# Kernel optimization log

Measured on AMD Instinct MI355X. Metric: run time of the kernel, lower is better.

Reference implementation:

```python
import jax, jax.numpy as jnp
import numpy as np

B, N, M = 2, 2048, 2048
D_K, D_V, H = 256, 256, 8
D_KS = D_K // H  # 32, per-head key dim (ceil(256/8))
D_VS = D_V // H  # 32
MASK_BIG = 1e32


def setup_inputs() -> dict:
    key = jax.random.key(0)
    ks = jax.random.split(key, 10)
    s = 0.02
    queries = jax.random.normal(ks[0], (B, N, D_K), jnp.float32)
    keys_ = jax.random.normal(ks[1], (B, M, D_K), jnp.float32)
    values = jax.random.normal(ks[2], (B, M, D_V), jnp.float32)
    presence = (jax.random.uniform(ks[3], (B, M)) > 0.3).astype(jnp.float32)
    Wq = jax.random.normal(ks[4], (D_K, D_KS * H), jnp.float32) * s
    bq = jnp.zeros((D_KS * H,), jnp.float32)
    Wk = jax.random.normal(ks[5], (D_K, D_KS * H), jnp.float32) * s
    bk = jnp.zeros((D_KS * H,), jnp.float32)
    Wv = jax.random.normal(ks[6], (D_V, D_VS * H), jnp.float32) * s
    bv = jnp.zeros((D_VS * H,), jnp.float32)
    Wo = jax.random.normal(ks[7], (D_VS * H, D_V), jnp.float32) * s
    bo = jnp.zeros((D_V,), jnp.float32)
    return {"queries": queries, "keys": keys_, "values": values, "presence": presence,
            "Wq": Wq, "bq": bq, "Wk": Wk, "bk": bk, "Wv": Wv, "bv": bv, "Wo": Wo, "bo": bo}


def reference(queries, keys, values, presence, Wq, bq, Wk, bk, Wv, bv, Wo, bo):
    # Project and split into heads. torch's split(d_k_s,-1)+cat(...,0) puts the
    # head index as the outer batch dim; a [B,N,H,d] reshape is the same math.
    q = (queries @ Wq + bq).reshape(B, N, H, D_KS)
    k = (keys @ Wk + bk).reshape(B, M, H, D_KS)
    v = (values @ Wv + bv).reshape(B, M, H, D_VS)
    # Raw scores, additive presence mask, then scale by sqrt(per-head d_k)
    scores = jnp.einsum('bnhd,bmhd->bhnm', q, k)
    scores = scores - (1.0 - presence)[:, None, None, :] * MASK_BIG
    attn = jax.nn.softmax(scores / np.sqrt(D_KS).astype(np.float32), axis=-1)
    o = jnp.einsum('bhnm,bmhd->bnhd', attn, v).reshape(B, N, H * D_VS)
    return o @ Wo + bo
```

## Files before the change

kernel.cpp:

```cpp
#include <hip/hip_runtime.h>

#define B_ 2
#define N_ 2048
#define M_ 2048
#define D_ 256
#define H_ 8
#define DH_ 32
#define SPLITS 2
#define QSCALE (0.17677669529663689f * 1.4426950408889634f)

typedef __attribute__((ext_vector_type(8))) short short8;
typedef __attribute__((ext_vector_type(4))) float f32x4;
typedef unsigned short u16;
typedef unsigned int u32;

#if __has_builtin(__builtin_amdgcn_exp2f)
#define EXP2 __builtin_amdgcn_exp2f
#else
#define EXP2 exp2f
#endif

__device__ __forceinline__ u16 f2bf(float f) {
  u32 u = __float_as_uint(f);
  return (u16)((u + 0x7fffu + ((u >> 16) & 1u)) >> 16);
}
__device__ __forceinline__ u32 cvtpk_bf16(float lo, float hi) {
  u32 r;
  asm("v_cvt_pk_bf16_f32 %0, %1, %2" : "=v"(r) : "v"(lo), "v"(hi));
  return r;
}
__device__ __forceinline__ void gload_lds16(const u16* g, u16* l) {
  __builtin_amdgcn_global_load_lds((const __attribute__((address_space(1))) void*)g,
                                   (__attribute__((address_space(3))) void*)l, 16, 0, 0);
}

__global__ __launch_bounds__(256, 2) void qkvproj_kernel(
    const float* __restrict__ Xq, const float* __restrict__ Xk, const float* __restrict__ Xv,
    const float* __restrict__ Wq, const float* __restrict__ Wk, const float* __restrict__ Wv,
    const float* __restrict__ bq, const float* __restrict__ bk, const float* __restrict__ bv,
    u16* __restrict__ qb, u16* __restrict__ kb, u16* __restrict__ vtb) {
  __shared__ u16 wsT[64 * 256];
  __shared__ u16 xs[64 * 256];
  const int p = blockIdx.y;
  const int nb = blockIdx.x & 63, cb = blockIdx.x >> 6;
  const int n0B = nb * 64, c0B = cb * 64;
  const float* X = p == 0 ? Xq : (p == 1 ? Xk : Xv);
  const float* W = p == 0 ? Wq : (p == 1 ? Wk : Wv);
  const float* bias = p == 0 ? bq : (p == 1 ? bk : bv);
  const int t = threadIdx.x;

  {
    const int cL = (t & 15) * 4, kB = (t >> 4) * 16;
    const float* wp = W + (size_t)kB * D_ + c0B + cL;
#pragma unroll
    for (int u = 0; u < 4; ++u) {
      const int k0 = kB + 4 * u;
      const f32x4 w0 = *(const f32x4*)(wp + (size_t)(4 * u + 0) * D_);
      const f32x4 w1 = *(const f32x4*)(wp + (size_t)(4 * u + 1) * D_);
      const f32x4 w2 = *(const f32x4*)(wp + (size_t)(4 * u + 2) * D_);
      const f32x4 w3 = *(const f32x4*)(wp + (size_t)(4 * u + 3) * D_);
#pragma unroll
      for (int cc = 0; cc < 4; ++cc) {
        const int c = cL + cc;
        uint2 v;
        v.x = cvtpk_bf16(w0[cc], w1[cc]);
        v.y = cvtpk_bf16(w2[cc], w3[cc]);
        *(uint2*)(wsT + c * 256 + (((k0 >> 3) ^ (c & 7)) * 8) + (k0 & 7)) = v;
      }
    }
  }
  {
    const int nL = t >> 2, k64 = (t & 3) * 64;
    const float* xp = X + (size_t)(n0B + nL) * D_ + k64;
#pragma unroll
    for (int m = 0; m < 8; ++m) {
      const f32x4 a = *(const f32x4*)(xp + 8 * m);
      const f32x4 b = *(const f32x4*)(xp + 8 * m + 4);
      uint4 v;
      v.x = cvtpk_bf16(a[0], a[1]);
      v.y = cvtpk_bf16(a[2], a[3]);
      v.z = cvtpk_bf16(b[0], b[1]);
      v.w = cvtpk_bf16(b[2], b[3]);
      const int k0 = k64 + 8 * m;
      *(uint4*)(xs + nL * 256 + (((k0 >> 3) ^ (nL & 7)) * 8)) = v;
    }
  }
  __syncthreads();

  const int wv = t >> 6, lane = t & 63, lr = lane & 15, lg = lane >> 4;
  const f32x4 zz = {0.f, 0.f, 0.f, 0.f};
  f32x4 acc[4] = {zz, zz, zz, zz};
  const int arow = wv * 16 + lr;
#pragma unroll
  for (int ks = 0; ks < 8; ++ks) {
    const short8 a = *(const short8*)(wsT + arow * 256 + (((ks * 4 + lg) ^ (arow & 7)) * 8));
#pragma unroll
    for (int ng = 0; ng < 4; ++ng) {
      const int brow = ng * 16 + lr;
      const short8 b = *(const short8*)(xs + brow * 256 + (((ks * 4 + lg) ^ (brow & 7)) * 8));
      acc[ng] = __builtin_amdgcn_mfma_f32_16x16x32_bf16(a, b, acc[ng], 0, 0, 0);
    }
  }

  const int cg4 = c0B + wv * 16 + lg * 4;
  const f32x4 bias4 = *(const f32x4*)(bias + cg4);
  if (p < 2) {
    u16* ob = p == 0 ? qb : kb;
    const float sc = p == 0 ? QSCALE : 1.0f;
#pragma unroll
    for (int ng = 0; ng < 4; ++ng) {
      const int n = n0B + ng * 16 + lr;
      const int b = n >> 11, nn = n & (N_ - 1);
#pragma unroll
      for (int j = 0; j < 4; ++j) {
        const int c = cg4 + j;
        ob[((size_t)(b * H_ + (c >> 5)) * N_ + nn) * DH_ + (c & 31)] =
            f2bf((acc[ng][j] + bias4[j]) * sc);
      }
    }
  } else {
#pragma unroll
    for (int ng = 0; ng < 4; ++ng) {
      const int n = n0B + ng * 16 + lr;
      const int b = n >> 11, nn = n & (M_ - 1);
#pragma unroll
      for (int j = 0; j < 4; ++j) {
        const int c = cg4 + j;
        vtb[((size_t)(b * H_ + (c >> 5)) * DH_ + (c & 31)) * M_ + nn] =
            f2bf(acc[ng][j] + bias4[j]);
      }
    }
  }
}

__global__ __launch_bounds__(256, 4) void attn_kernel(
    const u16* __restrict__ qb, const u16* __restrict__ kb,
    const u16* __restrict__ vtb, const float* __restrict__ presence,
    float* __restrict__ opart, float* __restrict__ lpart) {
  __shared__ u16 kvlds[2][4096];
  __shared__ u16 plds[4][1024];
  const int t = threadIdx.x;
  const int wv = t >> 6, lane = t & 63;
  const int lr = lane & 15, lg = lane >> 4;
  const int s = blockIdx.x >> 9;
  const int bh = (blockIdx.x >> 5) & 15;
  const int qblk = blockIdx.x & 31;
  const int b = bh >> 3, h = bh & 7;
  const int n0 = qblk * 64 + wv * 16;
  const int m0 = s * (M_ / SPLITS);
  const int NI = (M_ / SPLITS) / 64;

  const int gsk = (t & 3) ^ ((t >> 3) & 3);
  const u16* kst = kb + ((size_t)bh * M_ + m0 + (t >> 2)) * DH_ + gsk * 8;
  const int gsv = (t & 7) ^ ((t >> 3) & 7);
  const u16* vst = vtb + ((size_t)bh * DH_ + (t >> 3)) * M_ + m0 + gsv * 8;
  u16* const ldswK = &kvlds[0][0] + wv * 512;
  u16* const ldswV = &kvlds[0][0] + 2048 + wv * 512;

  const int ko0 = lr * 32 + (lg ^ ((lr >> 1) & 3)) * 8;
  const int sw = lr & 7;
  const int vo0 = (lg ^ sw) * 8;
  const int vo1 = ((4 + lg) ^ sw) * 8;

  const short8 qf = *(const short8*)(qb + ((size_t)bh * N_ + n0 + lr) * DH_ + lg * 8);
  const float* pbase = presence + (size_t)b * M_ + m0 + lg * 4;
  u16* const plw = plds[wv] + lr * 64;

  const f32x4 zz = {0.f, 0.f, 0.f, 0.f};
  f32x4 o0 = zz, o1 = zz, racc = zz;

  gload_lds16(kst, ldswK);
  gload_lds16(vst, ldswV);
  __syncthreads();

#pragma unroll 2
  for (int i = 0; i < NI; ++i) {
    const int mm = i * 64;
    const u16* kl = &kvlds[i & 1][0];
    const u16* vl = &kvlds[i & 1][2048];
    f32x4 pr[4];
#pragma unroll
    for (int tt = 0; tt < 4; ++tt) pr[tt] = *(const f32x4*)(pbase + mm + tt * 16);
    if (i + 1 < NI) {
      const int bo = ((i + 1) & 1) * 4096;
      gload_lds16(kst + (size_t)(i + 1) * (64 * DH_), ldswK + bo);
      gload_lds16(vst + (size_t)(i + 1) * 64, ldswV + bo);
    }

    f32x4 s4[4];
    __builtin_amdgcn_s_setprio(1);
#pragma unroll
    for (int tt = 0; tt < 4; ++tt) {
      const short8 kf = *(const short8*)(kl + tt * 512 + ko0);
      s4[tt] = __builtin_amdgcn_mfma_f32_16x16x32_bf16(kf, qf, zz, 0, 0, 0);
    }
    __builtin_amdgcn_s_setprio(0);

#pragma unroll
    for (int tt = 0; tt < 4; ++tt) {
      s4[tt] += (pr[tt] - 1.f) * 1e30f;
#pragma unroll
      for (int j = 0; j < 4; ++j) s4[tt][j] = EXP2(s4[tt][j]);
      racc += s4[tt];
      const int slot = (2 * tt + (lg >> 1)) ^ sw;
      *(uint2*)(plw + slot * 8 + (lg & 1) * 4) =
          make_uint2(cvtpk_bf16(s4[tt][0], s4[tt][1]), cvtpk_bf16(s4[tt][2], s4[tt][3]));
    }
    const short8 pf0 = *(const short8*)(plw + vo0);
    const short8 pf1 = *(const short8*)(plw + vo1);
    const short8 vf0 = *(const short8*)(vl + lr * 64 + vo0);
    const short8 vf1 = *(const short8*)(vl + lr * 64 + vo1);
    const short8 vf2 = *(const short8*)(vl + (16 + lr) * 64 + vo0);
    const short8 vf3 = *(const short8*)(vl + (16 + lr) * 64 + vo1);
    __builtin_amdgcn_s_setprio(1);
    o0 = __builtin_amdgcn_mfma_f32_16x16x32_bf16(pf0, vf0, o0, 0, 0, 0);
    o0 = __builtin_amdgcn_mfma_f32_16x16x32_bf16(pf1, vf1, o0, 0, 0, 0);
    o1 = __builtin_amdgcn_mfma_f32_16x16x32_bf16(pf0, vf2, o1, 0, 0, 0);
    o1 = __builtin_amdgcn_mfma_f32_16x16x32_bf16(pf1, vf3, o1, 0, 0, 0);
    __builtin_amdgcn_s_setprio(0);
    __syncthreads();
  }

  float l = (racc[0] + racc[1]) + (racc[2] + racc[3]);
  l += __shfl_xor(l, 16);
  l += __shfl_xor(l, 32);
  if (lg == 0) lpart[((size_t)s * (B_ * N_) + b * N_ + n0 + lr) * H_ + h] = l;

  float* ob = opart + ((size_t)s * (B_ * N_) + (size_t)b * N_ + n0) * D_ + h * DH_;
#pragma unroll
  for (int j = 0; j < 4; ++j) {
    const int q = lg * 4 + j;
    ob[(size_t)q * D_ + lr] = o0[j];
    ob[(size_t)q * D_ + 16 + lr] = o1[j];
  }
}

__global__ __launch_bounds__(256, 2) void projo_kernel(
    const float* __restrict__ opart, const float* __restrict__ lpart,
    const float* __restrict__ Wo, const float* __restrict__ bo,
    float* __restrict__ out) {
  __shared__ u16 wsT[64 * 256];
  __shared__ u16 xs[64 * 256];
  const int nb = blockIdx.x & 63, cb = blockIdx.x >> 6;
  const int n0B = nb * 64, c0B = cb * 64;
  const int t = threadIdx.x;

  {
    const int cL = (t & 15) * 4, kB = (t >> 4) * 16;
    const float* wp = Wo + (size_t)kB * D_ + c0B + cL;
#pragma unroll
    for (int u = 0; u < 4; ++u) {
      const int k0 = kB + 4 * u;
      const f32x4 w0 = *(const f32x4*)(wp + (size_t)(4 * u + 0) * D_);
      const f32x4 w1 = *(const f32x4*)(wp + (size_t)(4 * u + 1) * D_);
      const f32x4 w2 = *(const f32x4*)(wp + (size_t)(4 * u + 2) * D_);
      const f32x4 w3 = *(const f32x4*)(wp + (size_t)(4 * u + 3) * D_);
#pragma unroll
      for (int cc = 0; cc < 4; ++cc) {
        const int c = cL + cc;
        uint2 v;
        v.x = cvtpk_bf16(w0[cc], w1[cc]);
        v.y = cvtpk_bf16(w2[cc], w3[cc]);
        *(uint2*)(wsT + c * 256 + (((k0 >> 3) ^ (c & 7)) * 8) + (k0 & 7)) = v;
      }
    }
  }
  {
    const int nL = t >> 2, k64 = (t & 3) * 64;
    const int gn = n0B + nL;
    const float* o0p = opart + (size_t)gn * D_ + k64;
    const float* o1p = o0p + (size_t)(B_ * N_) * D_;
    const int h0 = k64 >> 5;
    const float il0 = 1.f / (lpart[(size_t)gn * H_ + h0] +
                             lpart[((size_t)(B_ * N_) + gn) * H_ + h0]);
    const float il1 = 1.f / (lpart[(size_t)gn * H_ + h0 + 1] +
                             lpart[((size_t)(B_ * N_) + gn) * H_ + h0 + 1]);
#pragma unroll
    for (int m = 0; m < 8; ++m) {
      f32x4 a = *(const f32x4*)(o0p + 8 * m) + *(const f32x4*)(o1p + 8 * m);
      f32x4 b = *(const f32x4*)(o0p + 8 * m + 4) + *(const f32x4*)(o1p + 8 * m + 4);
      const float il = (m < 4) ? il0 : il1;
      a *= il;
      b *= il;
      uint4 v;
      v.x = cvtpk_bf16(a[0], a[1]);
      v.y = cvtpk_bf16(a[2], a[3]);
      v.z = cvtpk_bf16(b[0], b[1]);
      v.w = cvtpk_bf16(b[2], b[3]);
      const int k0 = k64 + 8 * m;
      *(uint4*)(xs + nL * 256 + (((k0 >> 3) ^ (nL & 7)) * 8)) = v;
    }
  }
  __syncthreads();

  const int wv = t >> 6, lane = t & 63, lr = lane & 15, lg = lane >> 4;
  const f32x4 zz = {0.f, 0.f, 0.f, 0.f};
  f32x4 acc[4] = {zz, zz, zz, zz};
  const int arow = wv * 16 + lr;
#pragma unroll
  for (int ks = 0; ks < 8; ++ks) {
    const short8 a = *(const short8*)(xs + arow * 256 + (((ks * 4 + lg) ^ (arow & 7)) * 8));
#pragma unroll
    for (int ng = 0; ng < 4; ++ng) {
      const int brow = ng * 16 + lr;
      const short8 bfr = *(const short8*)(wsT + brow * 256 + (((ks * 4 + lg) ^ (brow & 7)) * 8));
      acc[ng] = __builtin_amdgcn_mfma_f32_16x16x32_bf16(a, bfr, acc[ng], 0, 0, 0);
    }
  }
#pragma unroll
  for (int ng = 0; ng < 4; ++ng) {
    const int c = c0B + ng * 16 + lr;
    const float bb = bo[c];
#pragma unroll
    for (int j = 0; j < 4; ++j)
      out[(size_t)(n0B + wv * 16 + lg * 4 + j) * D_ + c] = acc[ng][j] + bb;
  }
}

extern "C" void kernel_launch(void* const* d_in, const int* in_sizes, int n_in,
                              void* d_out, int out_size, void* d_ws, size_t ws_size,
                              hipStream_t stream) {
  (void)in_sizes; (void)n_in; (void)out_size; (void)ws_size;
  const float* queries  = (const float*)d_in[0];
  const float* keys     = (const float*)d_in[1];
  const float* values   = (const float*)d_in[2];
  const float* presence = (const float*)d_in[3];
  const float* Wq = (const float*)d_in[4];
  const float* bq = (const float*)d_in[5];
  const float* Wk = (const float*)d_in[6];
  const float* bk = (const float*)d_in[7];
  const float* Wv = (const float*)d_in[8];
  const float* bv = (const float*)d_in[9];
  const float* Wo = (const float*)d_in[10];
  const float* bo = (const float*)d_in[11];

  u16* qb  = (u16*)d_ws;
  u16* kb  = qb + (size_t)B_ * H_ * N_ * DH_;
  u16* vtb = kb + (size_t)B_ * H_ * M_ * DH_;
  float* opart = (float*)(vtb + (size_t)B_ * H_ * DH_ * M_);
  float* lpart = opart + (size_t)SPLITS * B_ * N_ * D_;

  qkvproj_kernel<<<dim3(256, 3), 256, 0, stream>>>(
      queries, keys, values, Wq, Wk, Wv, bq, bk, bv, qb, kb, vtb);
  attn_kernel<<<SPLITS * 16 * 32, 256, 0, stream>>>(qb, kb, vtb, presence, opart, lpart);
  projo_kernel<<<256, 256, 0, stream>>>(opart, lpart, Wo, bo, (float*)d_out);
}
```

Baseline: 47.57 us.

## Pre-transpose weights to bf16, retile projections, stage presence mask in LDS

Adds a small kernel that converts and transposes all four weight matrices to bf16 once per call. The QKV and output projection kernels then take 16-row tiles over all 256 output columns and read B fragments straight from global memory, instead of re-converting a weight tile into LDS in every block. The attention kernel remaps block indices, stages the presence row in LDS, and applies the mask as a multiply after exp2 instead of an additive -1e30 bias. The cost is an extra kernel launch and uncached-layout global reads of the weights, and the multiplicative mask behaves differently if every key is masked.

Result: slower. 54.63 us (+14.8%).

```diff
diff --git a/kernel.cpp b/kernel.cpp
--- a/kernel.cpp
+++ b/kernel.cpp
@@ -33,102 +33,117 @@
   __builtin_amdgcn_global_load_lds((const __attribute__((address_space(1))) void*)g,
                                    (__attribute__((address_space(3))) void*)l, 16, 0, 0);
 }
-
-__global__ __launch_bounds__(256, 2) void qkvproj_kernel(
+__device__ __forceinline__ void gload_lds16f(const float* g, float* l) {
+  __builtin_amdgcn_global_load_lds((const __attribute__((address_space(1))) void*)g,
+                                   (__attribute__((address_space(3))) void*)l, 16, 0, 0);
+}
+
+__global__ __launch_bounds__(256) void wtconv_kernel(
+    const float* __restrict__ Wq, const float* __restrict__ Wk,
+    const float* __restrict__ Wv, const float* __restrict__ Wo,
+    u16* __restrict__ wTq, u16* __restrict__ wTk, u16* __restrict__ wTv,
+    u16* __restrict__ wTo) {
+  __shared__ u16 sh[64][72];
+  const int blk = blockIdx.x;
+  const int mi = blk >> 4, tile = blk & 15;
+  const float* Ws = mi == 0 ? Wq : mi == 1 ? Wk : mi == 2 ? Wv : Wo;
+  u16* Wd = mi == 0 ? wTq : mi == 1 ? wTk : mi == 2 ? wTv : wTo;
+  const int r0 = (tile >> 2) * 64, c0 = (tile & 3) * 64;
+  const int r = threadIdx.x & 63, qt = threadIdx.x >> 6;
+  const float* sp = Ws + (size_t)(r0 + r) * D_ + c0 + qt * 16;
+  u32 w[8];
+#pragma unroll
+  for (int i = 0; i < 4; ++i) {
+    f32x4 v = *(const f32x4*)(sp + i * 4);
+    w[i * 2 + 0] = cvtpk_bf16(v[0], v[1]);
+    w[i * 2 + 1] = cvtpk_bf16(v[2], v[3]);
+  }
+  *(uint4*)(&sh[r][qt * 16]) = *(uint4*)&w[0];
+  *(uint4*)(&sh[r][qt * 16 + 8]) = *(uint4*)&w[4];
+  __syncthreads();
+  const int cc = threadIdx.x & 63;
+  u32 t2[8];
+#pragma unroll
+  for (int i = 0; i < 8; ++i) {
+    u32 lo = sh[qt * 16 + 2 * i][cc];
+    u32 hi = sh[qt * 16 + 2 * i + 1][cc];
+    t2[i] = lo | (hi << 16);
+  }
+  u16* op = Wd + (size_t)(c0 + cc) * D_ + r0 + qt * 16;
+  *(uint4*)op = *(uint4*)&t2[0];
+  *(uint4*)(op + 8) = *(uint4*)&t2[4];
+}
+
+__global__ __launch_bounds__(256, 4) void qkvproj_kernel(
     const float* __restrict__ Xq, const float* __restrict__ Xk, const float* __restrict__ Xv,
-    const float* __restrict__ Wq, const float* __restrict__ Wk, const float* __restrict__ Wv,
+    const u16* __restrict__ wTq, const u16* __restrict__ wTk, const u16* __restrict__ wTv,
     const float* __restrict__ bq, const float* __restrict__ bk, const float* __restrict__ bv,
     u16* __restrict__ qb, u16* __restrict__ kb, u16* __restrict__ vtb) {
-  __shared__ u16 wsT[64 * 256];
-  __shared__ u16 xs[64 * 256];
+  __shared__ u16 xs[16 * 256];
   const int p = blockIdx.y;
-  const int nb = blockIdx.x & 63, cb = blockIdx.x >> 6;
-  const int n0B = nb * 64, c0B = cb * 64;
+  const int n0 = blockIdx.x * 16;
   const float* X = p == 0 ? Xq : (p == 1 ? Xk : Xv);
-  const float* W = p == 0 ? Wq : (p == 1 ? Wk : Wv);
+  const u16* wT = p == 0 ? wTq : (p == 1 ? wTk : wTv);
   const float* bias = p == 0 ? bq : (p == 1 ? bk : bv);
   const int t = threadIdx.x;
 
   {
-    const int cL = (t & 15) * 4, kB = (t >> 4) * 16;
-    const float* wp = W + (size_t)kB * D_ + c0B + cL;
-#pragma unroll
-    for (int u = 0; u < 4; ++u) {
-      const int k0 = kB + 4 * u;
-      const f32x4 w0 = *(const f32x4*)(wp + (size_t)(4 * u + 0) * D_);
-      const f32x4 w1 = *(const f32x4*)(wp + (size_t)(4 * u + 1) * D_);
-      const f32x4 w2 = *(const f32x4*)(wp + (size_t)(4 * u + 2) * D_);
-      const f32x4 w3 = *(const f32x4*)(wp + (size_t)(4 * u + 3) * D_);
-#pragma unroll
-      for (int cc = 0; cc < 4; ++cc) {
-        const int c = cL + cc;
-        uint2 v;
-        v.x = cvtpk_bf16(w0[cc], w1[cc]);
-        v.y = cvtpk_bf16(w2[cc], w3[cc]);
-        *(uint2*)(wsT + c * 256 + (((k0 >> 3) ^ (c & 7)) * 8) + (k0 & 7)) = v;
-      }
-    }
-  }
-  {
-    const int nL = t >> 2, k64 = (t & 3) * 64;
-    const float* xp = X + (size_t)(n0B + nL) * D_ + k64;
-#pragma unroll
-    for (int m = 0; m < 8; ++m) {
+    const int nL = t >> 4, kc = (t & 15) * 16;
+    const float* xp = X + (size_t)(n0 + nL) * D_ + kc;
+#pragma unroll
+    for (int m = 0; m < 2; ++m) {
       const f32x4 a = *(const f32x4*)(xp + 8 * m);
-      const f32x4 b = *(const f32x4*)(xp + 8 * m + 4);
+      const f32x4 b2 = *(const f32x4*)(xp + 8 * m + 4);
       uint4 v;
       v.x = cvtpk_bf16(a[0], a[1]);
       v.y = cvtpk_bf16(a[2], a[3]);
-      v.z = cvtpk_bf16(b[0], b[1]);
-      v.w = cvtpk_bf16(b[2], b[3]);
-      const int k0 = k64 + 8 * m;
+      v.z = cvtpk_bf16(b2[0], b2[1]);
+      v.w = cvtpk_bf16(b2[2], b2[3]);
+      const int k0 = kc + 8 * m;
       *(uint4*)(xs + nL * 256 + (((k0 >> 3) ^ (nL & 7)) * 8)) = v;
     }
   }
   __syncthreads();
 
   const int wv = t >> 6, lane = t & 63, lr = lane & 15, lg = lane >> 4;
+  const int c0 = wv * 64;
   const f32x4 zz = {0.f, 0.f, 0.f, 0.f};
   f32x4 acc[4] = {zz, zz, zz, zz};
-  const int arow = wv * 16 + lr;
 #pragma unroll
   for (int ks = 0; ks < 8; ++ks) {
-    const short8 a = *(const short8*)(wsT + arow * 256 + (((ks * 4 + lg) ^ (arow & 7)) * 8));
-#pragma unroll
-    for (int ng = 0; ng < 4; ++ng) {
-      const int brow = ng * 16 + lr;
-      const short8 b = *(const short8*)(xs + brow * 256 + (((ks * 4 + lg) ^ (brow & 7)) * 8));
-      acc[ng] = __builtin_amdgcn_mfma_f32_16x16x32_bf16(a, b, acc[ng], 0, 0, 0);
-    }
-  }
-
-  const int cg4 = c0B + wv * 16 + lg * 4;
-  const f32x4 bias4 = *(const f32x4*)(bias + cg4);
+    const short8 a = *(const short8*)(xs + lr * 256 + (((ks * 4 + lg) ^ (lr & 7)) * 8));
+#pragma unroll
+    for (int ct = 0; ct < 4; ++ct) {
+      const short8 b = *(const short8*)(wT + (size_t)(c0 + ct * 16 + lr) * D_ + ks * 32 + lg * 8);
+      acc[ct] = __builtin_amdgcn_mfma_f32_16x16x32_bf16(a, b, acc[ct], 0, 0, 0);
+    }
+  }
+
+  const int bidx = n0 >> 11;
+  const int nn = (n0 & (N_ - 1)) + lg * 4;
   if (p < 2) {
     u16* ob = p == 0 ? qb : kb;
     const float sc = p == 0 ? QSCALE : 1.0f;
 #pragma unroll
-    for (int ng = 0; ng < 4; ++ng) {
-      const int n = n0B + ng * 16 + lr;
-      const int b = n >> 11, nn = n & (N_ - 1);
-#pragma unroll
-      for (int j = 0; j < 4; ++j) {
-        const int c = cg4 + j;
-        ob[((size_t)(b * H_ + (c >> 5)) * N_ + nn) * DH_ + (c & 31)] =
-            f2bf((acc[ng][j] + bias4[j]) * sc);
-      }
+    for (int ct = 0; ct < 4; ++ct) {
+      const int c = c0 + ct * 16 + lr;
+      const float bb = bias[c];
+      const int hh = c >> 5, dd = c & 31;
+#pragma unroll
+      for (int j = 0; j < 4; ++j)
+        ob[((size_t)(bidx * H_ + hh) * N_ + nn + j) * DH_ + dd] =
+            f2bf((acc[ct][j] + bb) * sc);
     }
   } else {
 #pragma unroll
-    for (int ng = 0; ng < 4; ++ng) {
-      const int n = n0B + ng * 16 + lr;
-      const int b = n >> 11, nn = n & (M_ - 1);
-#pragma unroll
-      for (int j = 0; j < 4; ++j) {
-        const int c = cg4 + j;
-        vtb[((size_t)(b * H_ + (c >> 5)) * DH_ + (c & 31)) * M_ + nn] =
-            f2bf(acc[ng][j] + bias4[j]);
-      }
+    for (int ct = 0; ct < 4; ++ct) {
+      const int c = c0 + ct * 16 + lr;
+      const float bb = bias[c];
+      const int hh = c >> 5, dd = c & 31;
+#pragma unroll
+      for (int j = 0; j < 4; ++j)
+        vtb[((size_t)(bidx * H_ + hh) * DH_ + dd) * M_ + nn + j] =
+            f2bf(acc[ct][j] + bb);
     }
   }
 }
@@ -139,12 +154,14 @@
     float* __restrict__ opart, float* __restrict__ lpart) {
   __shared__ u16 kvlds[2][4096];
   __shared__ u16 plds[4][1024];
+  __shared__ float prlds[1024];
   const int t = threadIdx.x;
   const int wv = t >> 6, lane = t & 63;
   const int lr = lane & 15, lg = lane >> 4;
-  const int s = blockIdx.x >> 9;
-  const int bh = (blockIdx.x >> 5) & 15;
-  const int qblk = blockIdx.x & 31;
+  const int g = blockIdx.x;
+  const int S = (g & 7) * 4 + ((g >> 3) & 3);
+  const int qblk = g >> 5;
+  const int s = S >> 4, bh = S & 15;
   const int b = bh >> 3, h = bh & 7;
   const int n0 = qblk * 64 + wv * 16;
   const int m0 = s * (M_ / SPLITS);
@@ -163,7 +180,6 @@
   const int vo1 = ((4 + lg) ^ sw) * 8;
 
   const short8 qf = *(const short8*)(qb + ((size_t)bh * N_ + n0 + lr) * DH_ + lg * 8);
-  const float* pbase = presence + (size_t)b * M_ + m0 + lg * 4;
   u16* const plw = plds[wv] + lr * 64;
 
   const f32x4 zz = {0.f, 0.f, 0.f, 0.f};
@@ -171,6 +187,7 @@
 
   gload_lds16(kst, ldswK);
   gload_lds16(vst, ldswV);
+  gload_lds16f(presence + (size_t)b * M_ + m0 + wv * 256 + lane * 4, prlds + wv * 256);
   __syncthreads();
 
 #pragma unroll 2
@@ -178,9 +195,6 @@
     const int mm = i * 64;
     const u16* kl = &kvlds[i & 1][0];
     const u16* vl = &kvlds[i & 1][2048];
-    f32x4 pr[4];
-#pragma unroll
-    for (int tt = 0; tt < 4; ++tt) pr[tt] = *(const f32x4*)(pbase + mm + tt * 16);
     if (i + 1 < NI) {
       const int bo = ((i + 1) & 1) * 4096;
       gload_lds16(kst + (size_t)(i + 1) * (64 * DH_), ldswK + bo);
@@ -198,9 +212,10 @@
 
 #pragma unroll
     for (int tt = 0; tt < 4; ++tt) {
-      s4[tt] += (pr[tt] - 1.f) * 1e30f;
+      const f32x4 pr = *(const f32x4*)(prlds + mm + tt * 16 + lg * 4);
 #pragma unroll
       for (int j = 0; j < 4; ++j) s4[tt][j] = EXP2(s4[tt][j]);
+      s4[tt] *= pr;
       racc += s4[tt];
       const int slot = (2 * tt + (lg >> 1)) ^ sw;
       *(uint2*)(plw + slot * 8 + (lg & 1) * 4) =
@@ -235,85 +250,59 @@
   }
 }
 
-__global__ __launch_bounds__(256, 2) void projo_kernel(
+__global__ __launch_bounds__(256, 4) void projo_kernel(
     const float* __restrict__ opart, const float* __restrict__ lpart,
-    const float* __restrict__ Wo, const float* __restrict__ bo,
+    const u16* __restrict__ wTo, const float* __restrict__ bo,
     float* __restrict__ out) {
-  __shared__ u16 wsT[64 * 256];
-  __shared__ u16 xs[64 * 256];
-  const int nb = blockIdx.x & 63, cb = blockIdx.x >> 6;
-  const int n0B = nb * 64, c0B = cb * 64;
+  __shared__ u16 xs[16 * 256];
+  const int n0 = blockIdx.x * 16;
   const int t = threadIdx.x;
 
   {
-    const int cL = (t & 15) * 4, kB = (t >> 4) * 16;
-    const float* wp = Wo + (size_t)kB * D_ + c0B + cL;
-#pragma unroll
-    for (int u = 0; u < 4; ++u) {
-      const int k0 = kB + 4 * u;
-      const f32x4 w0 = *(const f32x4*)(wp + (size_t)(4 * u + 0) * D_);
-      const f32x4 w1 = *(const f32x4*)(wp + (size_t)(4 * u + 1) * D_);
-      const f32x4 w2 = *(const f32x4*)(wp + (size_t)(4 * u + 2) * D_);
-      const f32x4 w3 = *(const f32x4*)(wp + (size_t)(4 * u + 3) * D_);
-#pragma unroll
-      for (int cc = 0; cc < 4; ++cc) {
-        const int c = cL + cc;
-        uint2 v;
-        v.x = cvtpk_bf16(w0[cc], w1[cc]);
-        v.y = cvtpk_bf16(w2[cc], w3[cc]);
-        *(uint2*)(wsT + c * 256 + (((k0 >> 3) ^ (c & 7)) * 8) + (k0 & 7)) = v;
-      }
-    }
-  }
-  {
-    const int nL = t >> 2, k64 = (t & 3) * 64;
-    const int gn = n0B + nL;
-    const float* o0p = opart + (size_t)gn * D_ + k64;
+    const int nL = t >> 4, kc = (t & 15) * 16;
+    const int gn = n0 + nL;
+    const float* o0p = opart + (size_t)gn * D_ + kc;
     const float* o1p = o0p + (size_t)(B_ * N_) * D_;
-    const int h0 = k64 >> 5;
-    const float il0 = 1.f / (lpart[(size_t)gn * H_ + h0] +
-                             lpart[((size_t)(B_ * N_) + gn) * H_ + h0]);
-    const float il1 = 1.f / (lpart[(size_t)gn * H_ + h0 + 1] +
-                             lpart[((size_t)(B_ * N_) + gn) * H_ + h0 + 1]);
-#pragma unroll
-    for (int m = 0; m < 8; ++m) {
+    const int h0 = kc >> 5;
+    const float il = 1.f / (lpart[(size_t)gn * H_ + h0] +
+                            lpart[((size_t)(B_ * N_) + gn) * H_ + h0]);
+#pragma unroll
+    for (int m = 0; m < 2; ++m) {
       f32x4 a = *(const f32x4*)(o0p + 8 * m) + *(const f32x4*)(o1p + 8 * m);
-      f32x4 b = *(const f32x4*)(o0p + 8 * m + 4) + *(const f32x4*)(o1p + 8 * m + 4);
-      const float il = (m < 4) ? il0 : il1;
+      f32x4 b2 = *(const f32x4*)(o0p + 8 * m + 4) + *(const f32x4*)(o1p + 8 * m + 4);
       a *= il;
-      b *= il;
+      b2 *= il;
       uint4 v;
       v.x = cvtpk_bf16(a[0], a[1]);
       v.y = cvtpk_bf16(a[2], a[3]);
-      v.z = cvtpk_bf16(b[0], b[1]);
-      v.w = cvtpk_bf16(b[2], b[3]);
-      const int k0 = k64 + 8 * m;
+      v.z = cvtpk_bf16(b2[0], b2[1]);
+      v.w = cvtpk_bf16(b2[2], b2[3]);
+      const int k0 = kc + 8 * m;
       *(uint4*)(xs + nL * 256 + (((k0 >> 3) ^ (nL & 7)) * 8)) = v;
     }
   }
   __syncthreads();
 
   const int wv = t >> 6, lane = t & 63, lr = lane & 15, lg = lane >> 4;
+  const int c0 = wv * 64;
   const f32x4 zz = {0.f, 0.f, 0.f, 0.f};
   f32x4 acc[4] = {zz, zz, zz, zz};
-  const int arow = wv * 16 + lr;
 #pragma unroll
   for (int ks = 0; ks < 8; ++ks) {
-    const short8 a = *(const short8*)(xs + arow * 256 + (((ks * 4 + lg) ^ (arow & 7)) * 8));
-#pragma unroll
-    for (int ng = 0; ng < 4; ++ng) {
-      const int brow = ng * 16 + lr;
-      const short8 bfr = *(const short8*)(wsT + brow * 256 + (((ks * 4 + lg) ^ (brow & 7)) * 8));
-      acc[ng] = __builtin_amdgcn_mfma_f32_16x16x32_bf16(a, bfr, acc[ng], 0, 0, 0);
-    }
-  }
-#pragma unroll
-  for (int ng = 0; ng < 4; ++ng) {
-    const int c = c0B + ng * 16 + lr;
+    const short8 a = *(const short8*)(xs + lr * 256 + (((ks * 4 + lg) ^ (lr & 7)) * 8));
+#pragma unroll
+    for (int ct = 0; ct < 4; ++ct) {
+      const short8 b = *(const short8*)(wTo + (size_t)(c0 + ct * 16 + lr) * D_ + ks * 32 + lg * 8);
+      acc[ct] = __builtin_amdgcn_mfma_f32_16x16x32_bf16(a, b, acc[ct], 0, 0, 0);
+    }
+  }
+#pragma unroll
+  for (int ct = 0; ct < 4; ++ct) {
+    const int c = c0 + ct * 16 + lr;
     const float bb = bo[c];
 #pragma unroll
     for (int j = 0; j < 4; ++j)
-      out[(size_t)(n0B + wv * 16 + lg * 4 + j) * D_ + c] = acc[ng][j] + bb;
+      out[(size_t)(n0 + lg * 4 + j) * D_ + c] = acc[ct][j] + bb;
   }
 }
 
@@ -334,14 +323,19 @@
   const float* Wo = (const float*)d_in[10];
   const float* bo = (const float*)d_in[11];
 
-  u16* qb  = (u16*)d_ws;
+  u16* wTq = (u16*)d_ws;
+  u16* wTk = wTq + 65536;
+  u16* wTv = wTk + 65536;
+  u16* wTo = wTv + 65536;
+  u16* qb  = wTo + 65536;
   u16* kb  = qb + (size_t)B_ * H_ * N_ * DH_;
   u16* vtb = kb + (size_t)B_ * H_ * M_ * DH_;
   float* opart = (float*)(vtb + (size_t)B_ * H_ * DH_ * M_);
   float* lpart = opart + (size_t)SPLITS * B_ * N_ * D_;
 
+  wtconv_kernel<<<64, 256, 0, stream>>>(Wq, Wk, Wv, Wo, wTq, wTk, wTv, wTo);
   qkvproj_kernel<<<dim3(256, 3), 256, 0, stream>>>(
-      queries, keys, values, Wq, Wk, Wv, bq, bk, bv, qb, kb, vtb);
+      queries, keys, values, wTq, wTk, wTv, bq, bk, bv, qb, kb, vtb);
   attn_kernel<<<SPLITS * 16 * 32, 256, 0, stream>>>(qb, kb, vtb, presence, opart, lpart);
-  projo_kernel<<<256, 256, 0, stream>>>(opart, lpart, Wo, bo, (float*)d_out);
-}
+  projo_kernel<<<256, 256, 0, stream>>>(opart, lpart, wTo, bo, (float*)d_out);
+}
```
